# Optimization experiments

Hardware: AMD Instinct MI355X
Metric: run time of the kernel (lower is better)

## Reference

```python
import jax, jax.numpy as jnp
import numpy as np

NUM_USERS = 100000
NUM_ITEMS = 50000
EMB = 64
NNZ = 4_800_000
N = NUM_USERS + NUM_ITEMS


def setup_inputs() -> dict:
    key = jax.random.key(0)
    k1, k2, k3, k4, k5 = jax.random.split(key, 5)
    row = jax.random.randint(k1, (NNZ,), 0, N, dtype=jnp.int64 if jax.config.jax_enable_x64 else jnp.int32)
    col = jax.random.randint(k2, (NNZ,), 0, N, dtype=row.dtype)
    # normalized adjacency values (positive, ~1/avg_degree scale)
    vals = jax.random.uniform(k3, (NNZ,), dtype=jnp.float32) * (1.0 / 32.0)
    user_emb = jax.random.normal(k4, (NUM_USERS, EMB), dtype=jnp.float32)
    item_emb = jax.random.normal(k5, (NUM_ITEMS, EMB), dtype=jnp.float32)
    return {"row": row, "col": col, "vals": vals,
            "user_emb": user_emb, "item_emb": item_emb, "n_layers": 3}


def reference(row, col, vals, user_emb, item_emb, n_layers):
    # ego_embeddings = cat(user, item)  -> [N, D]
    ego = jnp.concatenate([user_emb, item_emb], axis=0)
    acc = ego  # running sum over layers (layer 0 included)
    for _ in range(n_layers):
        # sparse.mm(norm_adj, ego): gather source rows, scale, scatter-add to dest rows
        ego = jax.ops.segment_sum(vals[:, None] * ego[col], row, num_segments=N)
        acc = acc + ego
    mean_emb = acc / jnp.asarray(n_layers + 1, dtype=acc.dtype)  # mean over layer axis
    return mean_emb[:NUM_USERS], mean_emb[NUM_USERS:]
```

## Files before the change

### kernel.cpp

```cpp
#include <hip/hip_runtime.h>
#include <hip/hip_fp16.h>


#define NUSERS 100000
#define NITEMS 50000
#define NN     150000
#define D      64
#define NNZ_E  4800000

#define NB_F   586
#define BU_PAD 592
#define NCHUNK 512
#define CH     9375
#define NSL    10
#define STAGE_CAP 12288

__global__ void init_kernel(const float* __restrict__ ue,
                            const float* __restrict__ ie,
                            __half* __restrict__ ego) {
    int t = blockIdx.x * blockDim.x + threadIdx.x;
    const int total = NN * (D / 4);
    if (t >= total) return;
    const int user_f4 = NUSERS * (D / 4);
    float4 v;
    if (t < user_f4) v = ((const float4*)ue)[t];
    else             v = ((const float4*)ie)[t - user_f4];
    __half2 h01 = __float22half2_rn(make_float2(v.x, v.y));
    __half2 h23 = __float22half2_rn(make_float2(v.z, v.w));
    uint2 packed;
    packed.x = *(unsigned*)&h01;
    packed.y = *(unsigned*)&h23;
    ((uint2*)ego)[t] = packed;
}

__global__ void p1_kernel(const int* __restrict__ row, int* __restrict__ cnt) {
    __shared__ int l[BU_PAD];
    for (int i = threadIdx.x; i < BU_PAD; i += 256) l[i] = 0;
    __syncthreads();
    int b = blockIdx.x;
    int beg = b * CH, end = min(beg + CH, NNZ_E);
    for (int e = beg + threadIdx.x; e < end; e += 256)
        atomicAdd(&l[row[e] >> 8], 1);
    __syncthreads();
    for (int i = threadIdx.x; i < BU_PAD; i += 256) cnt[b * BU_PAD + i] = l[i];
}

__global__ void s1_kernel(const int* __restrict__ cnt,
                          int* __restrict__ woff,
                          int* __restrict__ butot) {
    __shared__ int wsum[8];
    int bu = blockIdx.x;
    int c = threadIdx.x;
    int lane = c & 63;
    int w = c >> 6;
    int d = cnt[c * BU_PAD + bu];
    int incl = d;
    #pragma unroll
    for (int off = 1; off < 64; off <<= 1) {
        int t = __shfl_up(incl, off, 64);
        if (lane >= off) incl += t;
    }
    if (lane == 63) wsum[w] = incl;
    __syncthreads();
    int woffs = 0;
    for (int i = 0; i < w; ++i) woffs += wsum[i];
    woff[c * BU_PAD + bu] = woffs + incl - d;
    if (c == 511) butot[bu] = woffs + incl;
}

__global__ void s2_kernel(const int* __restrict__ butot, int* __restrict__ bbase) {
    __shared__ int sh[1024];
    int t = threadIdx.x;
    sh[t] = (t < NB_F) ? butot[t] : 0;
    __syncthreads();
    for (int off = 1; off < 1024; off <<= 1) {
        int x = (t >= off) ? sh[t - off] : 0;
        __syncthreads();
        sh[t] += x;
        __syncthreads();
    }
    if (t == 0) bbase[0] = 0;
    if (t < NB_F) bbase[t + 1] = sh[t];
}

__device__ __forceinline__ unsigned pack_cv(int c, float v) {
    unsigned code = (unsigned)(v * 524288.0f + 0.5f);
    code = min(code, 16383u);
    return ((unsigned)c << 14) | code;
}

__global__ void p2_kernel(const int* __restrict__ row,
                          const int* __restrict__ col,
                          const float* __restrict__ vals,
                          const int* __restrict__ woff,
                          const int* __restrict__ bbase,
                          uint2* __restrict__ rec) {
    __shared__ int cur[BU_PAD];
    int b = blockIdx.x;
    for (int i = threadIdx.x; i < BU_PAD; i += 256) {
        int base = (i < NB_F) ? bbase[i] : 0;
        cur[i] = base + woff[b * BU_PAD + i];
    }
    __syncthreads();
    int beg = b * CH, end = beg + CH;
    int e0 = beg + threadIdx.x;
    for (; e0 + 768 < end; e0 += 1024) {
        int r0 = row[e0];
        int r1 = row[e0 + 256];
        int r2 = row[e0 + 512];
        int r3 = row[e0 + 768];
        int c0 = col[e0];
        int c1 = col[e0 + 256];
        int c2 = col[e0 + 512];
        int c3 = col[e0 + 768];
        float v0 = vals[e0];
        float v1 = vals[e0 + 256];
        float v2 = vals[e0 + 512];
        float v3 = vals[e0 + 768];
        unsigned cv0 = pack_cv(c0, v0);
        unsigned cv1 = pack_cv(c1, v1);
        unsigned cv2 = pack_cv(c2, v2);
        unsigned cv3 = pack_cv(c3, v3);
        int p0 = atomicAdd(&cur[r0 >> 8], 1);
        int p1 = atomicAdd(&cur[r1 >> 8], 1);
        int p2 = atomicAdd(&cur[r2 >> 8], 1);
        int p3 = atomicAdd(&cur[r3 >> 8], 1);
        rec[p0] = make_uint2(cv0, (unsigned)(r0 & 255));
        rec[p1] = make_uint2(cv1, (unsigned)(r1 & 255));
        rec[p2] = make_uint2(cv2, (unsigned)(r2 & 255));
        rec[p3] = make_uint2(cv3, (unsigned)(r3 & 255));
    }
    for (; e0 < end; e0 += 256) {
        int r = row[e0];
        unsigned cv = pack_cv(col[e0], vals[e0]);
        int p = atomicAdd(&cur[r >> 8], 1);
        rec[p] = make_uint2(cv, (unsigned)(r & 255));
    }
}

__global__ __launch_bounds__(512) void p3f_kernel(const int* __restrict__ bbase,
                                                  const uint2* __restrict__ rec,
                                                  int* __restrict__ start,
                                                  int* __restrict__ deg,
                                                  unsigned* __restrict__ ecv) {
    __shared__ unsigned stage[STAGE_CAP];
    __shared__ int lh[256 * NSL];
    __shared__ int cur[256 * NSL];
    __shared__ int wsum[4];
    int bu = blockIdx.x;
    int beg = bbase[bu], end = bbase[bu + 1];
    int t = threadIdx.x;
    for (int i = t; i < 256 * NSL; i += 512) lh[i] = 0;
    __syncthreads();
    for (int i = beg + t; i < end; i += 512) {
        uint2 r = rec[i];
        atomicAdd(&lh[r.y * NSL + (r.x >> 28)], 1);
    }
    __syncthreads();
    int htot = 0, incl = 0;
    int lane = t & 63, w = t >> 6;
    if (t < 256) {
        #pragma unroll
        for (int s = 0; s < NSL; ++s) htot += lh[t * NSL + s];
        incl = htot;
        #pragma unroll
        for (int off = 1; off < 64; off <<= 1) {
            int x = __shfl_up(incl, off, 64);
            if (lane >= off) incl += x;
        }
        if (lane == 63) wsum[w] = incl;
    }
    __syncthreads();
    if (t < 256) {
        int woffs = 0;
        for (int i = 0; i < w; ++i) woffs += wsum[i];
        int excl = woffs + incl - htot;
        int run = excl;
        #pragma unroll
        for (int s = 0; s < NSL; ++s) {
            cur[t * NSL + s] = run;
            run += lh[t * NSL + s];
        }
        int n0 = (bu << 8) + t;
        if (n0 < NN) {
            start[n0] = beg + excl;
            deg[n0] = htot;
        }
    }
    __syncthreads();
    for (int i = beg + t; i < end; i += 512) {
        uint2 r = rec[i];
        int p = atomicAdd(&cur[r.y * NSL + (r.x >> 28)], 1);
        stage[p] = r.x;
    }
    __syncthreads();
    int n_edges = end - beg;
    for (int i = t; i < n_edges; i += 512)
        ecv[beg + i] = stage[i];
}

#define STEPG(rj, cj) do {                                             \
    float v_ = (float)((cj) & 16383u) * (1.0f / 524288.0f);            \
    const __half* h_ = (const __half*)&(rj);                           \
    sum[0] = fmaf(v_, __half2float(h_[0]), sum[0]);                    \
    sum[1] = fmaf(v_, __half2float(h_[1]), sum[1]);                    \
    sum[2] = fmaf(v_, __half2float(h_[2]), sum[2]);                    \
    sum[3] = fmaf(v_, __half2float(h_[3]), sum[3]);                    \
    sum[4] = fmaf(v_, __half2float(h_[4]), sum[4]);                    \
    sum[5] = fmaf(v_, __half2float(h_[5]), sum[5]);                    \
    sum[6] = fmaf(v_, __half2float(h_[6]), sum[6]);                    \
    sum[7] = fmaf(v_, __half2float(h_[7]), sum[7]);                    \
} while (0)

__global__ void gather_kernel(const int* __restrict__ start,
                              const int* __restrict__ deg,
                              const unsigned* __restrict__ ecv,
                              const __half* __restrict__ ego,
                              __half* __restrict__ nxt,
                              const __half* __restrict__ e1b,
                              const float* __restrict__ ue,
                              const float* __restrict__ ie,
                              float* __restrict__ acc,
                              int final_mode) {
    int wid = threadIdx.x >> 6;
    int lane = threadIdx.x & 63;
    int k = lane & 7;
    int g = lane >> 3;
    int n = blockIdx.x * 32 + wid * 8 + g;
    const float4* ego4 = (const float4*)ego;
    float sum[8] = {0.f, 0.f, 0.f, 0.f, 0.f, 0.f, 0.f, 0.f};

    int st = 0, dg = 0;
    if (n < NN) { st = start[n]; dg = deg[n]; }

    for (int e = 0; e < dg; e += 4) {
        unsigned c0 = ecv[st + e];
        unsigned c1 = (e + 1 < dg) ? ecv[st + e + 1] : 0u;
        unsigned c2 = (e + 2 < dg) ? ecv[st + e + 2] : 0u;
        unsigned c3 = (e + 3 < dg) ? ecv[st + e + 3] : 0u;
        float4 r0 = ego4[(c0 >> 14) * 8 + k];
        float4 r1 = ego4[(c1 >> 14) * 8 + k];
        float4 r2 = ego4[(c2 >> 14) * 8 + k];
        float4 r3 = ego4[(c3 >> 14) * 8 + k];
        STEPG(r0, c0);
        STEPG(r1, c1);
        STEPG(r2, c2);
        STEPG(r3, c3);
    }

    if (n >= NN) return;

    if (!final_mode) {
        __half2 h0 = __float22half2_rn(make_float2(sum[0], sum[1]));
        __half2 h1 = __float22half2_rn(make_float2(sum[2], sum[3]));
        __half2 h2 = __float22half2_rn(make_float2(sum[4], sum[5]));
        __half2 h3 = __float22half2_rn(make_float2(sum[6], sum[7]));
        uint4 packed;
        packed.x = *(unsigned*)&h0;
        packed.y = *(unsigned*)&h1;
        packed.z = *(unsigned*)&h2;
        packed.w = *(unsigned*)&h3;
        ((uint4*)nxt)[n * 8 + k] = packed;
    } else {
        int o = n * 16 + 2 * k;
        float4 a0, a1;
        if (n < NUSERS) {
            a0 = ((const float4*)ue)[o];
            a1 = ((const float4*)ue)[o + 1];
        } else {
            int m = (n - NUSERS) * 16 + 2 * k;
            a0 = ((const float4*)ie)[m];
            a1 = ((const float4*)ie)[m + 1];
        }
        uint4 p1v = ((const uint4*)e1b)[n * 8 + k];
        uint4 p2v = ((const uint4*)ego)[n * 8 + k];
        const __half2* e1h = (const __half2*)&p1v;
        const __half2* e2h = (const __half2*)&p2v;
        float2 e10 = __half22float2(e1h[0]), e11 = __half22float2(e1h[1]);
        float2 e12 = __half22float2(e1h[2]), e13 = __half22float2(e1h[3]);
        float2 e20 = __half22float2(e2h[0]), e21 = __half22float2(e2h[1]);
        float2 e22 = __half22float2(e2h[2]), e23 = __half22float2(e2h[3]);
        a0.x = 0.25f * (a0.x + e10.x + e20.x + sum[0]);
        a0.y = 0.25f * (a0.y + e10.y + e20.y + sum[1]);
        a0.z = 0.25f * (a0.z + e11.x + e21.x + sum[2]);
        a0.w = 0.25f * (a0.w + e11.y + e21.y + sum[3]);
        a1.x = 0.25f * (a1.x + e12.x + e22.x + sum[4]);
        a1.y = 0.25f * (a1.y + e12.y + e22.y + sum[5]);
        a1.z = 0.25f * (a1.z + e13.x + e23.x + sum[6]);
        a1.w = 0.25f * (a1.w + e13.y + e23.y + sum[7]);
        ((float4*)acc)[o] = a0;
        ((float4*)acc)[o + 1] = a1;
    }
}

extern "C" void kernel_launch(void* const* d_in, const int* in_sizes, int n_in,
                              void* d_out, int out_size, void* d_ws, size_t ws_size,
                              hipStream_t stream) {
    const int*   row  = (const int*)d_in[0];
    const int*   col  = (const int*)d_in[1];
    const float* vals = (const float*)d_in[2];
    const float* ue   = (const float*)d_in[3];
    const float* ie   = (const float*)d_in[4];

    float* acc = (float*)d_out;

    char* ws = (char*)d_ws;
    __half*   ego     = (__half*)(ws);
    __half*   nxt     = (__half*)(ws + (size_t)NN * D * 2);
    int*      cnt     = (int*)nxt;
    int*      woff    = cnt + (size_t)NCHUNK * BU_PAD;
    char*     p       = ws + 2 * (size_t)NN * D * 2;
    int*      start   = (int*)(p);              p += (size_t)NN * 4;
    int*      deg     = (int*)(p);              p += (size_t)NN * 4;
    int*      butot   = (int*)(p);              p += BU_PAD * 4;
    int*      bbase   = (int*)(p);              p += (NB_F + 8) * 4;
    unsigned* ecv     = (unsigned*)(p);         p += (size_t)NNZ_E * 4;
    uint2*    rec     = (uint2*)(p);

    const int f4_total = NN * (D / 4);
    const int init_blocks = (f4_total + 255) / 256;
    init_kernel<<<init_blocks, 256, 0, stream>>>(ue, ie, ego);

    p1_kernel<<<NCHUNK, 256, 0, stream>>>(row, cnt);
    s1_kernel<<<NB_F, 512, 0, stream>>>(cnt, woff, butot);
    s2_kernel<<<1, 1024, 0, stream>>>(butot, bbase);
    p2_kernel<<<NCHUNK, 256, 0, stream>>>(row, col, vals, woff, bbase, rec);
    p3f_kernel<<<NB_F, 512, 0, stream>>>(bbase, rec, start, deg, ecv);

    const int gather_blocks = (NN + 31) / 32;
    gather_kernel<<<gather_blocks, 256, 0, stream>>>(start, deg, ecv, ego, nxt,
                                                     (const __half*)0, ue, ie, acc, 0);
    gather_kernel<<<gather_blocks, 256, 0, stream>>>(start, deg, ecv, nxt, ego,
                                                     (const __half*)0, ue, ie, acc, 0);
    gather_kernel<<<gather_blocks, 256, 0, stream>>>(start, deg, ecv, ego, (\
__half*)0, nxt, ue, ie, acc, 1);
}
```

Baseline: 497.0 us.

## Sweep gather by column slices across node groups for source-row locality

Each destination row's edges are already sorted into NSL column slices (by the top bits of the packed col). The preprocessing now records per-slice cumulative counts per node, packed into a uint4. The gather is replaced by a persistent sweep kernel: 512 blocks each own a contiguous range of 293 nodes, and each thread group handles 5 nodes. The kernel walks the slices in order for all its nodes together, so concurrent gathers hit a narrower window of source rows and get better L2/MALL reuse. The cost is larger metadata (16 bytes per node), more loop overhead, and load imbalance from the fixed node partitioning. The 8-bit cumulative counts also overflow if a node has more than 255 edges.

```diff
diff --git a/kernel.cpp b/kernel.cpp
--- a/kernel.cpp
+++ b/kernel.cpp
@@ -14,6 +14,10 @@
 #define CH     9375
 #define NSL    10
 #define STAGE_CAP 12288
+
+#define SW_B   512
+#define SW_T   512
+#define NPB    293
 
 __global__ void init_kernel(const float* __restrict__ ue,
                             const float* __restrict__ ie,
@@ -141,7 +145,7 @@
 __global__ __launch_bounds__(512) void p3f_kernel(const int* __restrict__ bbase,
                                                   const uint2* __restrict__ rec,
                                                   int* __restrict__ start,
-                                                  int* __restrict__ deg,
+                                                  uint4* __restrict__ scum,
                                                   unsigned* __restrict__ ecv) {
     __shared__ unsigned stage[STAGE_CAP];
     __shared__ int lh[256 * NSL];
@@ -176,15 +180,21 @@
         for (int i = 0; i < w; ++i) woffs += wsum[i];
         int excl = woffs + incl - htot;
         int run = excl;
+        unsigned bx = 0, by = 0, bz = 0;
+        int rel = 0;
         #pragma unroll
         for (int s = 0; s < NSL; ++s) {
             cur[t * NSL + s] = run;
             run += lh[t * NSL + s];
+            rel += lh[t * NSL + s];
+            if (s < 4)      bx |= ((unsigned)rel) << (8 * s);
+            else if (s < 8) by |= ((unsigned)rel) << (8 * (s - 4));
+            else            bz |= ((unsigned)rel) << (8 * (s - 8));
         }
         int n0 = (bu << 8) + t;
         if (n0 < NN) {
             start[n0] = beg + excl;
-            deg[n0] = htot;
+            scum[n0] = make_uint4(bx, by, bz, (unsigned)htot);
         }
     }
     __syncthreads();
@@ -199,98 +209,135 @@
         ecv[beg + i] = stage[i];
 }
 
-#define STEPG(rj, cj) do {                                             \
+
+#define FMA8(sa, sb, rj, cj) do {                                      \
     float v_ = (float)((cj) & 16383u) * (1.0f / 524288.0f);            \
     const __half* h_ = (const __half*)&(rj);                           \
-    sum[0] = fmaf(v_, __half2float(h_[0]), sum[0]);                    \
-    sum[1] = fmaf(v_, __half2float(h_[1]), sum[1]);                    \
-    sum[2] = fmaf(v_, __half2float(h_[2]), sum[2]);                    \
-    sum[3] = fmaf(v_, __half2float(h_[3]), sum[3]);                    \
-    sum[4] = fmaf(v_, __half2float(h_[4]), sum[4]);                    \
-    sum[5] = fmaf(v_, __half2float(h_[5]), sum[5]);                    \
-    sum[6] = fmaf(v_, __half2float(h_[6]), sum[6]);                    \
-    sum[7] = fmaf(v_, __half2float(h_[7]), sum[7]);                    \
+    sa.x = fmaf(v_, __half2float(h_[0]), sa.x);                        \
+    sa.y = fmaf(v_, __half2float(h_[1]), sa.y);                        \
+    sa.z = fmaf(v_, __half2float(h_[2]), sa.z);                        \
+    sa.w = fmaf(v_, __half2float(h_[3]), sa.w);                        \
+    sb.x = fmaf(v_, __half2float(h_[4]), sb.x);                        \
+    sb.y = fmaf(v_, __half2float(h_[5]), sb.y);                        \
+    sb.z = fmaf(v_, __half2float(h_[6]), sb.z);                        \
+    sb.w = fmaf(v_, __half2float(h_[7]), sb.w);                        \
 } while (0)
 
-__global__ void gather_kernel(const int* __restrict__ start,
-                              const int* __restrict__ deg,
-                              const unsigned* __restrict__ ecv,
-                              const __half* __restrict__ ego,
-                              __half* __restrict__ nxt,
-                              const __half* __restrict__ e1b,
-                              const float* __restrict__ ue,
-                              const float* __restrict__ ie,
-                              float* __restrict__ acc,
-                              int final_mode) {
-    int wid = threadIdx.x >> 6;
-    int lane = threadIdx.x & 63;
-    int k = lane & 7;
-    int g = lane >> 3;
-    int n = blockIdx.x * 32 + wid * 8 + g;
+#define INIT_N(i)                                                      \
+    int n##i = base + (i) * 64 + g;                                    \
+    bool v##i = (n##i < lim);                                          \
+    int st##i = v##i ? start[n##i] : 0;                                \
+    uint4 mt##i = v##i ? scum[n##i] : make_uint4(0, 0, 0, 0);          \
+    int cur##i = st##i;                                                \
+    float4 sa##i = make_float4(0.f, 0.f, 0.f, 0.f);                    \
+    float4 sb##i = make_float4(0.f, 0.f, 0.f, 0.f);
+
+#define PROC(i) do {                                                   \
+    unsigned ws_ = (s < 4) ? mt##i.x : ((s < 8) ? mt##i.y : mt##i.z);  \
+    int en_ = st##i + (int)((ws_ >> ((s & 3) * 8)) & 255u);            \
+    while (cur##i < en_) {                                             \
+        int ce_ = cur##i;                                              \
+        unsigned c0 = ecv[ce_];                                        \
+        unsigned c1 = (ce_ + 1 < en_) ? ecv[ce_ + 1] : 0u;             \
+        unsigned c2 = (ce_ + 2 < en_) ? ecv[ce_ + 2] : 0u;             \
+        unsigned c3 = (ce_ + 3 < en_) ? ecv[ce_ + 3] : 0u;             \
+        float4 r0 = ego4[(c0 >> 14) * 8 + k];                          \
+        float4 r1 = ego4[(c1 >> 14) * 8 + k];                          \
+        float4 r2 = ego4[(c2 >> 14) * 8 + k];                          \
+        float4 r3 = ego4[(c3 >> 14) * 8 + k];                          \
+        FMA8(sa##i, sb##i, r0, c0);                                    \
+        FMA8(sa##i, sb##i, r1, c1);                                    \
+        FMA8(sa##i, sb##i, r2, c2);                                    \
+        FMA8(sa##i, sb##i, r3, c3);                                    \
+        cur##i += 4;                                                   \
+    }                                                                  \
+    cur##i = en_;                                                      \
+} while (0)
+
+#define EPI(i) do {                                                    \
+    if (v##i) {                                                        \
+        if (!final_mode) {                                             \
+            __half2 h0 = __float22half2_rn(make_float2(sa##i.x, sa##i.y)); \
+            __half2 h1 = __float22half2_rn(make_float2(sa##i.z, sa##i.w)); \
+            __half2 h2 = __float22half2_rn(make_float2(sb##i.x, sb##i.y)); \
+            __half2 h3 = __float22half2_rn(make_float2(sb##i.z, sb##i.w)); \
+            uint4 pk;                                                  \
+            pk.x = *(unsigned*)&h0;                                    \
+            pk.y = *(unsigned*)&h1;                                    \
+            pk.z = *(unsigned*)&h2;                                    \
+            pk.w = *(unsigned*)&h3;                                    \
+            ((uint4*)nxt)[n##i * 8 + k] = pk;                          \
+        } else {                                                       \
+            int o = n##i * 16 + 2 * k;                                 \
+            float4 a0, a1;                                             \
+            if (n##i < NUSERS) {                                       \
+                a0 = ((const float4*)ue)[o];                           \
+                a1 = ((const float4*)ue)[o + 1];                       \
+            } else {                                                   \
+                int m_ = (n##i - NUSERS) * 16 + 2 * k;                 \
+                a0 = ((const float4*)ie)[m_];                          \
+                a1 = ((const float4*)ie)[m_ + 1];                      \
+            }                                                          \
+            uint4 p1v = ((const uint4*)e1b)[n##i * 8 + k];             \
+            uint4 p2v = ((const uint4*)ego)[n##i * 8 + k];             \
+            const __half2* e1h = (const __half2*)&p1v;                 \
+            const __half2* e2h = (const __half2*)&p2v;                 \
+            float2 e10 = __half22float2(e1h[0]), e11 = __half22float2(e1h[1]); \
+            float2 e12 = __half22float2(e1h[2]), e13 = __half22float2(e1h[3]); \
+            float2 e20 = __half22float2(e2h[0]), e21 = __half22float2(e2h[1]); \
+            float2 e22 = __half22float2(e2h[2]), e23 = __half22float2(e2h[3]); \
+            a0.x = 0.25f * (a0.x + e10.x + e20.x + sa##i.x);           \
+            a0.y = 0.25f * (a0.y + e10.y + e20.y + sa##i.y);           \
+            a0.z = 0.25f * (a0.z + e11.x + e21.x + sa##i.z);           \
+            a0.w = 0.25f * (a0.w + e11.y + e21.y + sa##i.w);           \
+            a1.x = 0.25f * (a1.x + e12.x + e22.x + sb##i.x);           \
+            a1.y = 0.25f * (a1.y + e12.y + e22.y + sb##i.y);           \
+            a1.z = 0.25f * (a1.z + e13.x + e23.x + sb##i.z);           \
+            a1.w = 0.25f * (a1.w + e13.y + e23.y + sb##i.w);           \
+            ((float4*)acc)[o] = a0;                                    \
+            ((float4*)acc)[o + 1] = a1;                                \
+        }                                                              \
+    }                                                                  \
+} while (0)
+
+__global__ __launch_bounds__(SW_T, 4) void sweep_kernel(
+        const int* __restrict__ start,
+        const uint4* __restrict__ scum,
+        const unsigned* __restrict__ ecv,
+        const __half* __restrict__ ego,
+        __half* __restrict__ nxt,
+        const __half* __restrict__ e1b,
+        const float* __restrict__ ue,
+        const float* __restrict__ ie,
+        float* __restrict__ acc,
+        int final_mode) {
+    int tid = threadIdx.x;
+    int g = tid >> 3;
+    int k = tid & 7;
+    int base = blockIdx.x * NPB;
+    int lim = base + NPB;
+    if (lim > NN) lim = NN;
     const float4* ego4 = (const float4*)ego;
-    float sum[8] = {0.f, 0.f, 0.f, 0.f, 0.f, 0.f, 0.f, 0.f};
-
-    int st = 0, dg = 0;
-    if (n < NN) { st = start[n]; dg = deg[n]; }
-
-    for (int e = 0; e < dg; e += 4) {
-        unsigned c0 = ecv[st + e];
-        unsigned c1 = (e + 1 < dg) ? ecv[st + e + 1] : 0u;
-        unsigned c2 = (e + 2 < dg) ? ecv[st + e + 2] : 0u;
-        unsigned c3 = (e + 3 < dg) ? ecv[st + e + 3] : 0u;
-        float4 r0 = ego4[(c0 >> 14) * 8 + k];
-        float4 r1 = ego4[(c1 >> 14) * 8 + k];
-        float4 r2 = ego4[(c2 >> 14) * 8 + k];
-        float4 r3 = ego4[(c3 >> 14) * 8 + k];
-        STEPG(r0, c0);
-        STEPG(r1, c1);
-        STEPG(r2, c2);
-        STEPG(r3, c3);
-    }
-
-    if (n >= NN) return;
-
-    if (!final_mode) {
-        __half2 h0 = __float22half2_rn(make_float2(sum[0], sum[1]));
-        __half2 h1 = __float22half2_rn(make_float2(sum[2], sum[3]));
-        __half2 h2 = __float22half2_rn(make_float2(sum[4], sum[5]));
-        __half2 h3 = __float22half2_rn(make_float2(sum[6], sum[7]));
-        uint4 packed;
-        packed.x = *(unsigned*)&h0;
-        packed.y = *(unsigned*)&h1;
-        packed.z = *(unsigned*)&h2;
-        packed.w = *(unsigned*)&h3;
-        ((uint4*)nxt)[n * 8 + k] = packed;
-    } else {
-        int o = n * 16 + 2 * k;
-        float4 a0, a1;
-        if (n < NUSERS) {
-            a0 = ((const float4*)ue)[o];
-            a1 = ((const float4*)ue)[o + 1];
-        } else {
-            int m = (n - NUSERS) * 16 + 2 * k;
-            a0 = ((const float4*)ie)[m];
-            a1 = ((const float4*)ie)[m + 1];
-        }
-        uint4 p1v = ((const uint4*)e1b)[n * 8 + k];
-        uint4 p2v = ((const uint4*)ego)[n * 8 + k];
-        const __half2* e1h = (const __half2*)&p1v;
-        const __half2* e2h = (const __half2*)&p2v;
-        float2 e10 = __half22float2(e1h[0]), e11 = __half22float2(e1h[1]);
-        float2 e12 = __half22float2(e1h[2]), e13 = __half22float2(e1h[3]);
-        float2 e20 = __half22float2(e2h[0]), e21 = __half22float2(e2h[1]);
-        float2 e22 = __half22float2(e2h[2]), e23 = __half22float2(e2h[3]);
-        a0.x = 0.25f * (a0.x + e10.x + e20.x + sum[0]);
-        a0.y = 0.25f * (a0.y + e10.y + e20.y + sum[1]);
-        a0.z = 0.25f * (a0.z + e11.x + e21.x + sum[2]);
-        a0.w = 0.25f * (a0.w + e11.y + e21.y + sum[3]);
-        a1.x = 0.25f * (a1.x + e12.x + e22.x + sum[4]);
-        a1.y = 0.25f * (a1.y + e12.y + e22.y + sum[5]);
-        a1.z = 0.25f * (a1.z + e13.x + e23.x + sum[6]);
-        a1.w = 0.25f * (a1.w + e13.y + e23.y + sum[7]);
-        ((float4*)acc)[o] = a0;
-        ((float4*)acc)[o + 1] = a1;
-    }
+
+    INIT_N(0)
+    INIT_N(1)
+    INIT_N(2)
+    INIT_N(3)
+    INIT_N(4)
+
+    for (int s = 0; s < NSL; ++s) {
+        PROC(0);
+        PROC(1);
+        PROC(2);
+        PROC(3);
+        PROC(4);
+    }
+
+    EPI(0);
+    EPI(1);
+    EPI(2);
+    EPI(3);
+    EPI(4);
 }
 
 extern "C" void kernel_launch(void* const* d_in, const int* in_sizes, int n_in,
@@ -311,7 +358,7 @@
     int*      woff    = cnt + (size_t)NCHUNK * BU_PAD;
     char*     p       = ws + 2 * (size_t)NN * D * 2;
     int*      start   = (int*)(p);              p += (size_t)NN * 4;
-    int*      deg     = (int*)(p);              p += (size_t)NN * 4;
+    uint4*    scum    = (uint4*)(p);            p += (size_t)NN * 16;
     int*      butot   = (int*)(p);              p += BU_PAD * 4;
     int*      bbase   = (int*)(p);              p += (NB_F + 8) * 4;
     unsigned* ecv     = (unsigned*)(p);         p += (size_t)NNZ_E * 4;
@@ -325,13 +372,12 @@
     s1_kernel<<<NB_F, 512, 0, stream>>>(cnt, woff, butot);
     s2_kernel<<<1, 1024, 0, stream>>>(butot, bbase);
     p2_kernel<<<NCHUNK, 256, 0, stream>>>(row, col, vals, woff, bbase, rec);
-    p3f_kernel<<<NB_F, 512, 0, stream>>>(bbase, rec, start, deg, ecv);
-
-    const int gather_blocks = (NN + 31) / 32;
-    gather_kernel<<<gather_blocks, 256, 0, stream>>>(start, deg, ecv, ego, nxt,
-                                                     (const __half*)0, ue, ie, acc, 0);
-    gather_kernel<<<gather_blocks, 256, 0, stream>>>(start, deg, ecv, nxt, ego,
-                                                     (const __half*)0, ue, ie, acc, 0);
-    gather_kernel<<<gather_blocks, 256, 0, stream>>>(start, deg, ecv, ego, (\
-__half*)0, nxt, ue, ie, acc, 1);
-}
+    p3f_kernel<<<NB_F, 512, 0, stream>>>(bbase, rec, start, scum, ecv);
+
+    sweep_kernel<<<SW_B, SW_T, 0, stream>>>(start, scum, ecv, ego, nxt,
+                                            (const __half*)0, ue, ie, acc, 0);
+    sweep_kernel<<<SW_B, SW_T, 0, stream>>>(start, scum, ecv, nxt, ego,
+                                            (const __half*)0, ue, ie, acc, 0);
+    sweep_kernel<<<SW_B, SW_T, 0, stream>>>(start, scum, ecv, ego, (__half*)0,
+                                            nxt, ue, ie, acc, 1);
+}
```

New measurement: 536.8 us. +8.0%, slower.
